# Performance work log

Measured on AMD Instinct MI355X. Metric: run time of the kernel, lower is better.

Reference implementation:

```python
import jax, jax.numpy as jnp
import numpy as np

K = 3  # involution kernel size


def dwconv3x3(x, w, b):
    # x: [B,C,H,W], w: [C,1,3,3] (depthwise, groups=C), b: [C]
    y = jax.lax.conv_general_dilated(
        x, w, window_strides=(1, 1), padding='SAME',
        dimension_numbers=('NCHW', 'OIHW', 'NCHW'),
        feature_group_count=x.shape[1])
    return y + b[None, :, None, None]


def conv1x1(x, w, b):
    # x: [B,C,H,W], w: [O,C], b: [O]
    return jnp.einsum('oc,bchw->bohw', w, x) + b[None, :, None, None]


def extract_patches(x):
    # x: [B,C,H,W] -> [B,C,K*K,H,W], zero-padded 'same' 3x3 neighborhoods
    B, C, H, W = x.shape
    p = (K - 1) // 2
    xp = jnp.pad(x, ((0, 0), (0, 0), (p, p), (p, p)))
    return jnp.stack([xp[:, :, i:i + H, j:j + W]
                      for i in range(K) for j in range(K)], axis=2)


def involution(x, w_red, b_red, w_span, b_span):
    # dynamic per-pixel kernels: [B, K*K, H, W]
    kern = conv1x1(jax.nn.relu(conv1x1(x, w_red, b_red)), w_span, b_span)
    patches = extract_patches(x)                 # [B,C,KK,H,W]
    return jnp.einsum('bkhw,bckhw->bchw', kern, patches)


def setup_inputs() -> dict:
    key = jax.random.key(0)
    ks = jax.random.split(key, 10)
    dim, red = 256, 64  # reduction ratio 4
    B, H, W = 8, 64, 64
    s = 0.05
    return {
        'x': jax.random.normal(ks[0], (B, dim, H, W), jnp.float32),
        'w_in': jax.random.normal(ks[1], (dim, 1, 3, 3), jnp.float32) * s,
        'b_in': jax.random.normal(ks[2], (dim,), jnp.float32) * s,
        'w_red': jax.random.normal(ks[3], (red, dim), jnp.float32) * s,
        'b_red': jax.random.normal(ks[4], (red,), jnp.float32) * s,
        'w_span': jax.random.normal(ks[5], (K * K, red), jnp.float32) * s,
        'b_span': jax.random.normal(ks[6], (K * K,), jnp.float32) * s,
        'w_out': jax.random.normal(ks[7], (dim, 1, 3, 3), jnp.float32) * s,
        'b_out': jax.random.normal(ks[8], (dim,), jnp.float32) * s,
    }


def reference(x, w_in, b_in, w_red, b_red, w_span, b_span, w_out, b_out):
    x = dwconv3x3(x, w_in, b_in)
    x = involution(x, w_red, b_red, w_span, b_span)
    x = dwconv3x3(x, w_out, b_out)
    return x
```

## Files before the change

### kernel.cpp

```cpp
#include <hip/hip_runtime.h>

#define BB 8
#define CC 256
#define HH 64
#define WW 64
#define RED 64
#define HW 4096
#define AST 72
#define LSF 68
#define LSH 72

typedef __attribute__((ext_vector_type(8))) short s8v;
typedef __attribute__((ext_vector_type(4))) float f4v;

__device__ __forceinline__ unsigned short f2bf(float f) {
    unsigned u = __float_as_uint(f);
    u += 0x7fff + ((u >> 16) & 1);
    return (unsigned short)(u >> 16);
}
__device__ __forceinline__ float b2f(unsigned short u) {
    return __uint_as_float(((unsigned)u) << 16);
}

__global__ __launch_bounds__(256) void build_wtf(const float* __restrict__ w_red,
                                                 unsigned short* __restrict__ wtf) {
    int e = blockIdx.x * 256 + threadIdx.x;
    int j = e & 7, l = (e >> 3) & 63, nt = (e >> 9) & 3, kbg = e >> 11;
    int o = nt * 16 + (l & 15);
    int c = kbg * 32 + ((l >> 4) & 3) * 8 + j;
    wtf[e] = f2bf(w_red[o * CC + c]);
}

__global__ __launch_bounds__(256, 4) void dw_kern(const float* __restrict__ x,
                                                  const float* __restrict__ w_in,
                                                  const float* __restrict__ b_in,
                                                  const unsigned short* __restrict__ wtf,
                                                  const float* __restrict__ b_red,
                                                  const float* __restrict__ w_span,
                                                  const float* __restrict__ b_span,
                                                  float* __restrict__ kern,
                                                  unsigned short* __restrict__ x1g) {
    alignas(16) __shared__ char smem[8448 + 12288];
    unsigned short* xs = (unsigned short*)smem;
    float* r_lds = (float*)smem;
    float* wl    = (float*)(smem + 8448);
    float* part  = (float*)(smem + 8448);

    const int t    = threadIdx.x;
    const int bx   = blockIdx.x;
    const int band = bx & 7;
    const int idx  = bx >> 3;
    const int h    = band * 8 + (idx >> 1);
    const int wh   = idx & 1;
    const int b    = blockIdx.y;
    const int l  = t & 63;
    const int wv = t >> 6;
    const int mt = wv & 1, nh = wv >> 1;
    const int m0 = mt << 4;
    const int q  = t & 7;
    const int pl = q << 2;
    const int wg = (wh << 5) | pl;
    const int cr = t >> 3;

    #pragma unroll
    for (int j = 0; j < 9; j++) {
        int i = j * 256 + t;
        wl[(i / 9) * 12 + (i % 9)] = w_in[i];
    }
    wl[t * 12 + 9] = b_in[t];

    float4 pv[2][3]; float plf[2][3], prt[2][3];

    auto loadX = [&](int c0) {
        #pragma unroll
        for (int s = 0; s < 2; s++) {
            const int cc = c0 + s * 32 + cr;
            const float* xp = x + ((size_t)(b * CC + cc)) * HW;
            #pragma unroll
            for (int ky = 0; ky < 3; ky++) {
                int hh = h + ky - 1;
                if (hh < 0 || hh >= HH) {
                    pv[s][ky] = make_float4(0.f, 0.f, 0.f, 0.f);
                    plf[s][ky] = 0.f; prt[s][ky] = 0.f;
                    continue;
                }
                const float* row = xp + hh * WW + wg;
                pv[s][ky]  = *(const float4*)row;
                plf[s][ky] = (wg > 0)      ? row[-1] : 0.f;
                prt[s][ky] = (wg + 4 < WW) ? row[4]  : 0.f;
            }
        }
    };
    auto computeA = [&](int c0) {
        #pragma unroll
        for (int s = 0; s < 2; s++) {
            const int cl = s * 32 + cr;
            const int cc = c0 + cl;
            const float* wp = wl + cc * 12;
            float4 wa = *(const float4*)wp;
            float4 wb = *(const float4*)(wp + 4);
            float2 wc = *(const float2*)(wp + 8);
            float4 a4 = make_float4(wc.y, wc.y, wc.y, wc.y);
            const float kw[9] = {wa.x, wa.y, wa.z, wa.w, wb.x, wb.y, wb.z, wb.w, wc.x};
            #pragma unroll
            for (int ky = 0; ky < 3; ky++) {
                float4 v = pv[s][ky];
                float lf = plf[s][ky], rt = prt[s][ky];
                float k0 = kw[ky * 3 + 0], k1 = kw[ky * 3 + 1], k2 = kw[ky * 3 + 2];
                a4.x = fmaf(k0, lf,  a4.x); a4.y = fmaf(k0, v.x, a4.y);
                a4.z = fmaf(k0, v.y, a4.z); a4.w = fmaf(k0, v.z, a4.w);
                a4.x = fmaf(k1, v.x, a4.x); a4.y = fmaf(k1, v.y, a4.y);
                a4.z = fmaf(k1, v.z, a4.z); a4.w = fmaf(k1, v.w, a4.w);
                a4.x = fmaf(k2, v.y, a4.x); a4.y = fmaf(k2, v.z, a4.y);
                a4.z = fmaf(k2, v.w, a4.z); a4.w = fmaf(k2, rt,  a4.w);
            }
            ushort4 pk;
            pk.x = f2bf(a4.x); pk.y = f2bf(a4.y);
            pk.z = f2bf(a4.z); pk.w = f2bf(a4.w);
            xs[(pl + 0) * AST + cl] = pk.x;
            xs[(pl + 1) * AST + cl] = pk.y;
            xs[(pl + 2) * AST + cl] = pk.z;
            xs[(pl + 3) * AST + cl] = pk.w;
            *(ushort4*)(x1g + ((size_t)(b * CC + cc)) * HW + h * WW + wg) = pk;
        }
    };

    s8v bfr[2][2];
    auto loadB = [&](int k) {
        #pragma unroll
        for (int kb = 0; kb < 2; kb++)
            #pragma unroll
            for (int ntl = 0; ntl < 2; ntl++) {
                int nt = (nh << 1) + ntl;
                int kbg = (k << 1) + kb;
                bfr[kb][ntl] = *(const s8v*)(wtf + (((kbg * 4 + nt) * 64 + l) << 3));
            }
    };

    f4v acc[2] = {{0.f, 0.f, 0.f, 0.f}, {0.f, 0.f, 0.f, 0.f}};

    loadX(0); loadB(0);
    __syncthreads();
    for (int k = 0; k < 4; k++) {
        computeA(k << 6);
        if (k < 3) loadX((k + 1) << 6);
        __syncthreads();
        #pragma unroll
        for (int kb = 0; kb < 2; kb++) {
            const unsigned short* ap =
                xs + (m0 + (l & 15)) * AST + (kb << 5) + ((l >> 4) & 3) * 8;
            s8v av = *(const s8v*)ap;
            #pragma unroll
            for (int ntl = 0; ntl < 2; ntl++)
                acc[ntl] = __builtin_amdgcn_mfma_f32_16x16x32_bf16(
                    av, bfr[kb][ntl], acc[ntl], 0, 0, 0);
        }
        if (k < 3) loadB(k + 1);
        __syncthreads();
    }

    #pragma unroll
    for (int ntl = 0; ntl < 2; ntl++) {
        int o = ((nh << 1) + ntl) * 16 + (l & 15);
        int pxr = m0 + ((l >> 4) & 3) * 4;
        #pragma unroll
        for (int i = 0; i < 4; i++)
            r_lds[o * 33 + pxr + i] = acc[ntl][i];
    }
    __syncthreads();

    const int px = t & 31;
    const int og = t >> 5;
    const int o0 = og << 3;
    float kk[9];
    #pragma unroll
    for (int j = 0; j < 9; j++) kk[j] = 0.f;
    #pragma unroll
    for (int i = 0; i < 8; i++) {
        float r = fmaxf(r_lds[(o0 + i) * 33 + px] + b_red[o0 + i], 0.f);
        #pragma unroll
        for (int j = 0; j < 9; j++) kk[j] = fmaf(w_span[j * RED + o0 + i], r, kk[j]);
    }
    __syncthreads();
    #pragma unroll
    for (int j = 0; j < 9; j++) part[(og * 9 + j) * 32 + px] = kk[j];
    __syncthreads();

    float* kp = kern + (size_t)b * 9 * HW + h * WW + (wh << 5) + px;
    const int jj = t >> 5;
    {
        float s = b_span[jj];
        #pragma unroll
        for (int g = 0; g < 8; g++) s += part[(g * 9 + jj) * 32 + px];
        kp[jj * HW] = s;
    }
    if (t < 32) {
        float s = b_span[8];
        #pragma unroll
        for (int g = 0; g < 8; g++) s += part[(g * 9 + 8) * 32 + px];
        kp[8 * HW] = s;
    }
}

__global__ __launch_bounds__(256) void invol_dw(const unsigned short* __restrict__ x1g,
                                                const float* __restrict__ kern,
                                                const float* __restrict__ w_out,
                                                const float* __restrict__ b_out,
                                                float* __restrict__ out) {
    __shared__ unsigned short x1s[HH * LSH];
    __shared__ float res[HH * LSF];
    const int t  = threadIdx.x;
    const int q  = t & 15;
    const int w0 = q << 2;
    const int r  = t >> 4;
    const int c = blockIdx.x, b = blockIdx.y;

    {
        const unsigned short* xp = x1g + ((size_t)(b * CC + c)) * HW;
        const int hl = t >> 2;
        const int wl2 = (t & 3) << 4;
        *(s8v*)&x1s[hl * LSH + wl2]     = *(const s8v*)(xp + hl * WW + wl2);
        *(s8v*)&x1s[hl * LSH + wl2 + 8] = *(const s8v*)(xp + hl * WW + wl2 + 8);
    }
    __syncthreads();

    const float* kp = kern + (size_t)b * 9 * HW;
    #pragma unroll
    for (int i = 0; i < 4; i++) {
        int h  = r + (i << 4);
        int hw = h * WW + w0;
        float4 acc = make_float4(0.f, 0.f, 0.f, 0.f);
        #pragma unroll
        for (int ky = 0; ky < 3; ky++) {
            int hh = h + ky - 1;
            if (hh < 0 || hh >= HH) continue;
            const unsigned short* row = &x1s[hh * LSH + w0];
            float vx = b2f(row[0]), vy = b2f(row[1]);
            float vz = b2f(row[2]), vw = b2f(row[3]);
            float lf = (w0 > 0)      ? b2f(row[-1]) : 0.f;
            float rt = (w0 + 4 < WW) ? b2f(row[4])  : 0.f;
            float4 k0 = *(const float4*)(kp + (ky * 3 + 0) * HW + hw);
            float4 k1 = *(const float4*)(kp + (ky * 3 + 1) * HW + hw);
            float4 k2 = *(const float4*)(kp + (ky * 3 + 2) * HW + hw);
            acc.x = fmaf(k0.x, lf, acc.x); acc.y = fmaf(k0.y, vx, acc.y);
            acc.z = fmaf(k0.z, vy, acc.z); acc.w = fmaf(k0.w, vz, acc.w);
            acc.x = fmaf(k1.x, vx, acc.x); acc.y = fmaf(k1.y, vy, acc.y);
            acc.z = fmaf(k1.z, vz, acc.z); acc.w = fmaf(k1.w, vw, acc.w);
            acc.x = fmaf(k2.x, vy, acc.x); acc.y = fmaf(k2.y, vz, acc.y);
            acc.z = fmaf(k2.z, vw, acc.z); acc.w = fmaf(k2.w, rt, acc.w);
        }
        *(float4*)&res[h * LSF + w0] = acc;
    }
    __syncthreads();

    const float* wp = w_out + c * 9;
    const float bb = b_out[c];
    float* op = out + ((size_t)(b * CC + c)) * HW;
    #pragma unroll
    for (int i = 0; i < 4; i++) {
        int h = r + (i << 4);
        float4 acc = make_float4(bb, bb, bb, bb);
        #pragma unroll
        for (int ky = 0; ky < 3; ky++) {
            int hh = h + ky - 1;
            if (hh < 0 || hh >= HH) continue;
            const float* row = &res[hh * LSF + w0];
            float4 v = *(const float4*)row;
            float lf = (w0 > 0)      ? row[-1] : 0.f;
            float rt = (w0 + 4 < WW) ? row[4]  : 0.f;
            float k0 = wp[ky * 3 + 0], k1 = wp[ky * 3 + 1], k2 = wp[ky * 3 + 2];
            acc.x = fmaf(k0, lf,  acc.x); acc.y = fmaf(k0, v.x, acc.y);
            acc.z = fmaf(k0, v.y, acc.z); acc.w = fmaf(k0, v.z, acc.w);
            acc.x = fmaf(k1, v.x, acc.x); acc.y = fmaf(k1, v.y, acc.y);
            acc.z = fmaf(k1, v.z, acc.z); acc.w = fmaf(k1, v.w, acc.w);
            acc.x = fmaf(k2, v.y, acc.x); acc.y = fmaf(k2, v.z, acc.y);
            acc.z = fmaf(k2, v.w, acc.z); acc.w = fmaf(k2, rt,  acc.w);
        }
        *(float4*)(op + h * WW + w0) = acc;
    }
}

extern "C" void kernel_launch(void* const* d_in, const int* in_sizes, int n_in,
                              void* d_out, int out_size, void* d_ws, size_t ws_size,
                              hipStream_t stream) {
    const float* x      = (const float*)d_in[0];
    const float* w_in   = (const float*)d_in[1];
    const float* b_in   = (const float*)d_in[2];
    const float* w_red  = (const float*)d_in[3];
    const float* b_red  = (const float*)d_in[4];
    const float* w_span = (const float*)d_in[5];
    const float* b_span = (const float*)d_in[6];
    const float* w_out  = (const float*)d_in[7];
    const float* b_out  = (const float*)d_in[8];
    float* out = (float*)d_out;

    float* kern = (float*)d_ws;
    unsigned short* x1g = (unsigned short*)(kern + (size_t)BB * 9 * HW);
    unsigned short* wtf = x1g + (size_t)BB * CC * HW;

    build_wtf<<<64, 256, 0, stream>>>(w_red, wtf);
    dw_kern<<<dim3(128, BB), 256, 0, stream>>>(x, w_in, b_in, wtf, b_red,
                                               w_span, b_span, kern, x1g);
    invol_dw<<<dim3(CC, BB), 256, 0, stream>>>(x1g, kern, w_out, b_out, out);
}
```

Before: 138.1 us.

## Halve dw_kern pixel tile, shrink LDS, store involution intermediate as bf16

dw_kern now processes 16 pixels per block instead of 32, so it launches twice as many blocks. Each wave handles one MFMA tile, LDS use is reduced, and launch bounds are raised to allow more resident blocks, aiming at better latency hiding. invol_dw stores its intermediate involution result in LDS as bf16 instead of fp32, halving that buffer so more blocks fit per CU. The trade-offs are more redundant halo loads and duplicated weight staging per block, plus an extra bf16 rounding step before the output depthwise conv, which reduces precision.

```diff
diff --git a/kernel.cpp b/kernel.cpp
--- a/kernel.cpp
+++ b/kernel.cpp
@@ -7,8 +7,8 @@
 #define RED 64
 #define HW 4096
 #define AST 72
-#define LSF 68
 #define LSH 72
+#define WLS 10
 
 typedef __attribute__((ext_vector_type(8))) short s8v;
 typedef __attribute__((ext_vector_type(4))) float f4v;
@@ -31,7 +31,7 @@
     wtf[e] = f2bf(w_red[o * CC + c]);
 }
 
-__global__ __launch_bounds__(256, 4) void dw_kern(const float* __restrict__ x,
+__global__ __launch_bounds__(256, 8) void dw_kern(const float* __restrict__ x,
                                                   const float* __restrict__ w_in,
                                                   const float* __restrict__ b_in,
                                                   const unsigned short* __restrict__ wtf,
@@ -40,104 +40,89 @@
                                                   const float* __restrict__ b_span,
                                                   float* __restrict__ kern,
                                                   unsigned short* __restrict__ x1g) {
-    alignas(16) __shared__ char smem[8448 + 12288];
+    alignas(16) __shared__ char smem[4608 + 10240];
     unsigned short* xs = (unsigned short*)smem;
     float* r_lds = (float*)smem;
-    float* wl    = (float*)(smem + 8448);
-    float* part  = (float*)(smem + 8448);
+    float* wl    = (float*)(smem + 4608);
+    float* part  = (float*)(smem + 4608);
 
     const int t    = threadIdx.x;
     const int bx   = blockIdx.x;
     const int band = bx & 7;
     const int idx  = bx >> 3;
-    const int h    = band * 8 + (idx >> 1);
-    const int wh   = idx & 1;
+    const int h    = band * 8 + (idx >> 2);
+    const int qh   = idx & 3;
     const int b    = blockIdx.y;
     const int l  = t & 63;
     const int wv = t >> 6;
-    const int mt = wv & 1, nh = wv >> 1;
-    const int m0 = mt << 4;
-    const int q  = t & 7;
+    const int q  = t & 3;
     const int pl = q << 2;
-    const int wg = (wh << 5) | pl;
-    const int cr = t >> 3;
+    const int wg = (qh << 4) | pl;
+    const int cr = t >> 2;
 
     #pragma unroll
     for (int j = 0; j < 9; j++) {
         int i = j * 256 + t;
-        wl[(i / 9) * 12 + (i % 9)] = w_in[i];
-    }
-    wl[t * 12 + 9] = b_in[t];
-
-    float4 pv[2][3]; float plf[2][3], prt[2][3];
+        wl[(i / 9) * WLS + (i % 9)] = w_in[i];
+    }
+    wl[t * WLS + 9] = b_in[t];
+
+    float4 pv[3]; float plf[3], prt[3];
 
     auto loadX = [&](int c0) {
-        #pragma unroll
-        for (int s = 0; s < 2; s++) {
-            const int cc = c0 + s * 32 + cr;
-            const float* xp = x + ((size_t)(b * CC + cc)) * HW;
-            #pragma unroll
-            for (int ky = 0; ky < 3; ky++) {
-                int hh = h + ky - 1;
-                if (hh < 0 || hh >= HH) {
-                    pv[s][ky] = make_float4(0.f, 0.f, 0.f, 0.f);
-                    plf[s][ky] = 0.f; prt[s][ky] = 0.f;
-                    continue;
-                }
-                const float* row = xp + hh * WW + wg;
-                pv[s][ky]  = *(const float4*)row;
-                plf[s][ky] = (wg > 0)      ? row[-1] : 0.f;
-                prt[s][ky] = (wg + 4 < WW) ? row[4]  : 0.f;
+        const int cc = c0 + cr;
+        const float* xp = x + ((size_t)(b * CC + cc)) * HW;
+        #pragma unroll
+        for (int ky = 0; ky < 3; ky++) {
+            int hh = h + ky - 1;
+            if (hh < 0 || hh >= HH) {
+                pv[ky] = make_float4(0.f, 0.f, 0.f, 0.f);
+                plf[ky] = 0.f; prt[ky] = 0.f;
+                continue;
             }
+            const float* row = xp + hh * WW + wg;
+            pv[ky]  = *(const float4*)row;
+            plf[ky] = (wg > 0)      ? row[-1] : 0.f;
+            prt[ky] = (wg + 4 < WW) ? row[4]  : 0.f;
         }
     };
     auto computeA = [&](int c0) {
-        #pragma unroll
-        for (int s = 0; s < 2; s++) {
-            const int cl = s * 32 + cr;
-            const int cc = c0 + cl;
-            const float* wp = wl + cc * 12;
-            float4 wa = *(const float4*)wp;
-            float4 wb = *(const float4*)(wp + 4);
-            float2 wc = *(const float2*)(wp + 8);
-            float4 a4 = make_float4(wc.y, wc.y, wc.y, wc.y);
-            const float kw[9] = {wa.x, wa.y, wa.z, wa.w, wb.x, wb.y, wb.z, wb.w, wc.x};
-            #pragma unroll
-            for (int ky = 0; ky < 3; ky++) {
-                float4 v = pv[s][ky];
-                float lf = plf[s][ky], rt = prt[s][ky];
-                float k0 = kw[ky * 3 + 0], k1 = kw[ky * 3 + 1], k2 = kw[ky * 3 + 2];
-                a4.x = fmaf(k0, lf,  a4.x); a4.y = fmaf(k0, v.x, a4.y);
-                a4.z = fmaf(k0, v.y, a4.z); a4.w = fmaf(k0, v.z, a4.w);
-                a4.x = fmaf(k1, v.x, a4.x); a4.y = fmaf(k1, v.y, a4.y);
-                a4.z = fmaf(k1, v.z, a4.z); a4.w = fmaf(k1, v.w, a4.w);
-                a4.x = fmaf(k2, v.y, a4.x); a4.y = fmaf(k2, v.z, a4.y);
-                a4.z = fmaf(k2, v.w, a4.z); a4.w = fmaf(k2, rt,  a4.w);
-            }
-            ushort4 pk;
-            pk.x = f2bf(a4.x); pk.y = f2bf(a4.y);
-            pk.z = f2bf(a4.z); pk.w = f2bf(a4.w);
-            xs[(pl + 0) * AST + cl] = pk.x;
-            xs[(pl + 1) * AST + cl] = pk.y;
-            xs[(pl + 2) * AST + cl] = pk.z;
-            xs[(pl + 3) * AST + cl] = pk.w;
-            *(ushort4*)(x1g + ((size_t)(b * CC + cc)) * HW + h * WW + wg) = pk;
-        }
+        const int cc = c0 + cr;
+        const float* wp = wl + cc * WLS;
+        const float bb = wp[9];
+        float4 a4 = make_float4(bb, bb, bb, bb);
+        #pragma unroll
+        for (int ky = 0; ky < 3; ky++) {
+            float4 v = pv[ky];
+            float lf = plf[ky], rt = prt[ky];
+            float k0 = wp[ky * 3 + 0], k1 = wp[ky * 3 + 1], k2 = wp[ky * 3 + 2];
+            a4.x = fmaf(k0, lf,  a4.x); a4.y = fmaf(k0, v.x, a4.y);
+            a4.z = fmaf(k0, v.y, a4.z); a4.w = fmaf(k0, v.z, a4.w);
+            a4.x = fmaf(k1, v.x, a4.x); a4.y = fmaf(k1, v.y, a4.y);
+            a4.z = fmaf(k1, v.z, a4.z); a4.w = fmaf(k1, v.w, a4.w);
+            a4.x = fmaf(k2, v.y, a4.x); a4.y = fmaf(k2, v.z, a4.y);
+            a4.z = fmaf(k2, v.w, a4.z); a4.w = fmaf(k2, rt,  a4.w);
+        }
+        ushort4 pk;
+        pk.x = f2bf(a4.x); pk.y = f2bf(a4.y);
+        pk.z = f2bf(a4.z); pk.w = f2bf(a4.w);
+        xs[(pl + 0) * AST + cr] = pk.x;
+        xs[(pl + 1) * AST + cr] = pk.y;
+        xs[(pl + 2) * AST + cr] = pk.z;
+        xs[(pl + 3) * AST + cr] = pk.w;
+        *(ushort4*)(x1g + ((size_t)(b * CC + cc)) * HW + h * WW + wg) = pk;
     };
 
-    s8v bfr[2][2];
+    s8v bfr[2];
     auto loadB = [&](int k) {
         #pragma unroll
-        for (int kb = 0; kb < 2; kb++)
-            #pragma unroll
-            for (int ntl = 0; ntl < 2; ntl++) {
-                int nt = (nh << 1) + ntl;
-                int kbg = (k << 1) + kb;
-                bfr[kb][ntl] = *(const s8v*)(wtf + (((kbg * 4 + nt) * 64 + l) << 3));
-            }
+        for (int kb = 0; kb < 2; kb++) {
+            int kbg = (k << 1) + kb;
+            bfr[kb] = *(const s8v*)(wtf + (((kbg * 4 + wv) * 64 + l) << 3));
+        }
     };
 
-    f4v acc[2] = {{0.f, 0.f, 0.f, 0.f}, {0.f, 0.f, 0.f, 0.f}};
+    f4v acc = {0.f, 0.f, 0.f, 0.f};
 
     loadX(0); loadB(0);
     __syncthreads();
@@ -148,67 +133,56 @@
         #pragma unroll
         for (int kb = 0; kb < 2; kb++) {
             const unsigned short* ap =
-                xs + (m0 + (l & 15)) * AST + (kb << 5) + ((l >> 4) & 3) * 8;
+                xs + (l & 15) * AST + (kb << 5) + ((l >> 4) & 3) * 8;
             s8v av = *(const s8v*)ap;
-            #pragma unroll
-            for (int ntl = 0; ntl < 2; ntl++)
-                acc[ntl] = __builtin_amdgcn_mfma_f32_16x16x32_bf16(
-                    av, bfr[kb][ntl], acc[ntl], 0, 0, 0);
+            acc = __builtin_amdgcn_mfma_f32_16x16x32_bf16(av, bfr[kb], acc, 0, 0, 0);
         }
         if (k < 3) loadB(k + 1);
         __syncthreads();
     }
 
-    #pragma unroll
-    for (int ntl = 0; ntl < 2; ntl++) {
-        int o = ((nh << 1) + ntl) * 16 + (l & 15);
-        int pxr = m0 + ((l >> 4) & 3) * 4;
+    {
+        int o = (wv << 4) + (l & 15);
+        int pxr = ((l >> 4) & 3) * 4;
         #pragma unroll
         for (int i = 0; i < 4; i++)
-            r_lds[o * 33 + pxr + i] = acc[ntl][i];
-    }
-    __syncthreads();
-
-    const int px = t & 31;
-    const int og = t >> 5;
-    const int o0 = og << 3;
+            r_lds[o * 17 + pxr + i] = acc[i];
+    }
+    __syncthreads();
+
+    const int px = t & 15;
+    const int og = t >> 4;
+    const int o0 = og << 2;
     float kk[9];
     #pragma unroll
     for (int j = 0; j < 9; j++) kk[j] = 0.f;
     #pragma unroll
-    for (int i = 0; i < 8; i++) {
-        float r = fmaxf(r_lds[(o0 + i) * 33 + px] + b_red[o0 + i], 0.f);
+    for (int i = 0; i < 4; i++) {
+        float r = fmaxf(r_lds[(o0 + i) * 17 + px] + b_red[o0 + i], 0.f);
         #pragma unroll
         for (int j = 0; j < 9; j++) kk[j] = fmaf(w_span[j * RED + o0 + i], r, kk[j]);
     }
     __syncthreads();
     #pragma unroll
-    for (int j = 0; j < 9; j++) part[(og * 9 + j) * 32 + px] = kk[j];
-    __syncthreads();
-
-    float* kp = kern + (size_t)b * 9 * HW + h * WW + (wh << 5) + px;
-    const int jj = t >> 5;
-    {
+    for (int j = 0; j < 9; j++) part[(og * 9 + j) * 16 + px] = kk[j];
+    __syncthreads();
+
+    if (t < 144) {
+        const int jj = t >> 4;
         float s = b_span[jj];
         #pragma unroll
-        for (int g = 0; g < 8; g++) s += part[(g * 9 + jj) * 32 + px];
-        kp[jj * HW] = s;
-    }
-    if (t < 32) {
-        float s = b_span[8];
-        #pragma unroll
-        for (int g = 0; g < 8; g++) s += part[(g * 9 + 8) * 32 + px];
-        kp[8 * HW] = s;
-    }
-}
-
-__global__ __launch_bounds__(256) void invol_dw(const unsigned short* __restrict__ x1g,
-                                                const float* __restrict__ kern,
-                                                const float* __restrict__ w_out,
-                                                const float* __restrict__ b_out,
-                                                float* __restrict__ out) {
+        for (int g = 0; g < 16; g++) s += part[(g * 9 + jj) * 16 + px];
+        kern[(size_t)b * 9 * HW + jj * HW + h * WW + (qh << 4) + px] = s;
+    }
+}
+
+__global__ __launch_bounds__(256, 8) void invol_dw(const unsigned short* __restrict__ x1g,
+                                                   const float* __restrict__ kern,
+                                                   const float* __restrict__ w_out,
+                                                   const float* __restrict__ b_out,
+                                                   float* __restrict__ out) {
     __shared__ unsigned short x1s[HH * LSH];
-    __shared__ float res[HH * LSF];
+    __shared__ unsigned short res[HH * LSH];
     const int t  = threadIdx.x;
     const int q  = t & 15;
     const int w0 = q << 2;
@@ -249,7 +223,10 @@
             acc.x = fmaf(k2.x, vy, acc.x); acc.y = fmaf(k2.y, vz, acc.y);
             acc.z = fmaf(k2.z, vw, acc.z); acc.w = fmaf(k2.w, rt, acc.w);
         }
-        *(float4*)&res[h * LSF + w0] = acc;
+        ushort4 pk;
+        pk.x = f2bf(acc.x); pk.y = f2bf(acc.y);
+        pk.z = f2bf(acc.z); pk.w = f2bf(acc.w);
+        *(ushort4*)&res[h * LSH + w0] = pk;
     }
     __syncthreads();
 
@@ -264,17 +241,18 @@
         for (int ky = 0; ky < 3; ky++) {
             int hh = h + ky - 1;
             if (hh < 0 || hh >= HH) continue;
-            const float* row = &res[hh * LSF + w0];
-            float4 v = *(const float4*)row;
-            float lf = (w0 > 0)      ? row[-1] : 0.f;
-            float rt = (w0 + 4 < WW) ? row[4]  : 0.f;
+            const unsigned short* row = &res[hh * LSH + w0];
+            float vx = b2f(row[0]), vy = b2f(row[1]);
+            float vz = b2f(row[2]), vw = b2f(row[3]);
+            float lf = (w0 > 0)      ? b2f(row[-1]) : 0.f;
+            float rt = (w0 + 4 < WW) ? b2f(row[4])  : 0.f;
             float k0 = wp[ky * 3 + 0], k1 = wp[ky * 3 + 1], k2 = wp[ky * 3 + 2];
-            acc.x = fmaf(k0, lf,  acc.x); acc.y = fmaf(k0, v.x, acc.y);
-            acc.z = fmaf(k0, v.y, acc.z); acc.w = fmaf(k0, v.z, acc.w);
-            acc.x = fmaf(k1, v.x, acc.x); acc.y = fmaf(k1, v.y, acc.y);
-            acc.z = fmaf(k1, v.z, acc.z); acc.w = fmaf(k1, v.w, acc.w);
-            acc.x = fmaf(k2, v.y, acc.x); acc.y = fmaf(k2, v.z, acc.y);
-            acc.z = fmaf(k2, v.w, acc.z); acc.w = fmaf(k2, rt,  acc.w);
+            acc.x = fmaf(k0, lf, acc.x); acc.y = fmaf(k0, vx, acc.y);
+            acc.z = fmaf(k0, vy, acc.z); acc.w = fmaf(k0, vz, acc.w);
+            acc.x = fmaf(k1, vx, acc.x); acc.y = fmaf(k1, vy, acc.y);
+            acc.z = fmaf(k1, vz, acc.z); acc.w = fmaf(k1, vw, acc.w);
+            acc.x = fmaf(k2, vy, acc.x); acc.y = fmaf(k2, vz, acc.y);
+            acc.z = fmaf(k2, vw, acc.z); acc.w = fmaf(k2, rt, acc.w);
         }
         *(float4*)(op + h * WW + w0) = acc;
     }
@@ -299,7 +277,7 @@
     unsigned short* wtf = x1g + (size_t)BB * CC * HW;
 
     build_wtf<<<64, 256, 0, stream>>>(w_red, wtf);
-    dw_kern<<<dim3(128, BB), 256, 0, stream>>>(x, w_in, b_in, wtf, b_red,
+    dw_kern<<<dim3(256, BB), 256, 0, stream>>>(x, w_in, b_in, wtf, b_red,
                                                w_span, b_span, kern, x1g);
     invol_dw<<<dim3(CC, BB), 256, 0, stream>>>(x1g, kern, w_out, b_out, out);
 }
```

Result: slower. 162.5 us (+17.6%).

## Coalesce x1 stores via LDS staging, shuffle halos, bf16 intermediate in invol_dw

Applied to the files above, without the earlier changes.

The first kernel now stages each bf16 x1 tile in shared memory and writes it to global as 16-byte vectors at the end, instead of issuing scattered 8-byte stores per channel. It also gets horizontal halo values through lane shuffles rather than extra global loads, and caches w_span, b_red and b_span in LDS. The second kernel keeps its intermediate result in LDS as bf16, halving that buffer so launch bounds can allow 8 blocks. The bf16 intermediate adds rounding error, and the first kernel's extra LDS use may lower its occupancy.

```diff
diff --git a/kernel.cpp b/kernel.cpp
--- a/kernel.cpp
+++ b/kernel.cpp
@@ -7,8 +7,9 @@
 #define RED 64
 #define HW 4096
 #define AST 72
-#define LSF 68
+#define XST 40
 #define LSH 72
+#define WLS 10
 
 typedef __attribute__((ext_vector_type(8))) short s8v;
 typedef __attribute__((ext_vector_type(4))) float f4v;
@@ -40,11 +41,15 @@
                                                   const float* __restrict__ b_span,
                                                   float* __restrict__ kern,
                                                   unsigned short* __restrict__ x1g) {
-    alignas(16) __shared__ char smem[8448 + 12288];
-    unsigned short* xs = (unsigned short*)smem;
-    float* r_lds = (float*)smem;
-    float* wl    = (float*)(smem + 8448);
-    float* part  = (float*)(smem + 8448);
+    alignas(16) __shared__ char smem[8448 + 5120 + 10240 + 2640];
+    unsigned short* xs  = (unsigned short*)smem;
+    float* r_lds        = (float*)smem;
+    unsigned short* xst = (unsigned short*)(smem + 8448);
+    float* wl           = (float*)(smem + 13568);
+    float* part         = (float*)(smem + 13568);
+    float* ws_l         = (float*)(smem + 23808);
+    float* br_l         = ws_l + 576;
+    float* bs_l         = br_l + 64;
 
     const int t    = threadIdx.x;
     const int bx   = blockIdx.x;
@@ -65,11 +70,15 @@
     #pragma unroll
     for (int j = 0; j < 9; j++) {
         int i = j * 256 + t;
-        wl[(i / 9) * 12 + (i % 9)] = w_in[i];
-    }
-    wl[t * 12 + 9] = b_in[t];
-
-    float4 pv[2][3]; float plf[2][3], prt[2][3];
+        wl[(i / 9) * WLS + (i % 9)] = w_in[i];
+    }
+    wl[t * WLS + 9] = b_in[t];
+    ws_l[t]       = w_span[t];
+    ws_l[256 + t] = w_span[256 + t];
+    if (t < 64) { ws_l[512 + t] = w_span[512 + t]; br_l[t] = b_red[t]; }
+    if (t < 9)  bs_l[t] = b_span[t];
+
+    float4 pv[2][3]; float phal[2][3];
 
     auto loadX = [&](int c0) {
         #pragma unroll
@@ -81,13 +90,15 @@
                 int hh = h + ky - 1;
                 if (hh < 0 || hh >= HH) {
                     pv[s][ky] = make_float4(0.f, 0.f, 0.f, 0.f);
-                    plf[s][ky] = 0.f; prt[s][ky] = 0.f;
+                    phal[s][ky] = 0.f;
                     continue;
                 }
                 const float* row = xp + hh * WW + wg;
-                pv[s][ky]  = *(const float4*)row;
-                plf[s][ky] = (wg > 0)      ? row[-1] : 0.f;
-                prt[s][ky] = (wg + 4 < WW) ? row[4]  : 0.f;
+                pv[s][ky] = *(const float4*)row;
+                float hv = 0.f;
+                if (q == 0) { if (wg > 0) hv = row[-1]; }
+                else if (q == 7) { if (wg + 4 < WW) hv = row[4]; }
+                phal[s][ky] = hv;
             }
         }
     };
@@ -96,17 +107,17 @@
         for (int s = 0; s < 2; s++) {
             const int cl = s * 32 + cr;
             const int cc = c0 + cl;
-            const float* wp = wl + cc * 12;
-            float4 wa = *(const float4*)wp;
-            float4 wb = *(const float4*)(wp + 4);
-            float2 wc = *(const float2*)(wp + 8);
-            float4 a4 = make_float4(wc.y, wc.y, wc.y, wc.y);
-            const float kw[9] = {wa.x, wa.y, wa.z, wa.w, wb.x, wb.y, wb.z, wb.w, wc.x};
+            const float* wp = wl + cc * WLS;
+            const float bb = wp[9];
+            float4 a4 = make_float4(bb, bb, bb, bb);
             #pragma unroll
             for (int ky = 0; ky < 3; ky++) {
                 float4 v = pv[s][ky];
-                float lf = plf[s][ky], rt = prt[s][ky];
-                float k0 = kw[ky * 3 + 0], k1 = kw[ky * 3 + 1], k2 = kw[ky * 3 + 2];
+                float lf = __shfl_up(v.w, 1);
+                if (q == 0) lf = phal[s][ky];
+                float rt = __shfl_down(v.x, 1);
+                if (q == 7) rt = phal[s][ky];
+                float k0 = wp[ky * 3 + 0], k1 = wp[ky * 3 + 1], k2 = wp[ky * 3 + 2];
                 a4.x = fmaf(k0, lf,  a4.x); a4.y = fmaf(k0, v.x, a4.y);
                 a4.z = fmaf(k0, v.y, a4.z); a4.w = fmaf(k0, v.z, a4.w);
                 a4.x = fmaf(k1, v.x, a4.x); a4.y = fmaf(k1, v.y, a4.y);
@@ -121,7 +132,7 @@
             xs[(pl + 1) * AST + cl] = pk.y;
             xs[(pl + 2) * AST + cl] = pk.z;
             xs[(pl + 3) * AST + cl] = pk.w;
-            *(ushort4*)(x1g + ((size_t)(b * CC + cc)) * HW + h * WW + wg) = pk;
+            *(ushort4*)&xst[cl * XST + pl] = pk;
         }
     };
 
@@ -138,6 +149,9 @@
     };
 
     f4v acc[2] = {{0.f, 0.f, 0.f, 0.f}, {0.f, 0.f, 0.f, 0.f}};
+    int4 x1r[4];
+    const int c2  = t >> 2;
+    const int px2 = (t & 3) << 3;
 
     loadX(0); loadB(0);
     __syncthreads();
@@ -155,6 +169,7 @@
                 acc[ntl] = __builtin_amdgcn_mfma_f32_16x16x32_bf16(
                     av, bfr[kb][ntl], acc[ntl], 0, 0, 0);
         }
+        x1r[k] = *(const int4*)&xst[c2 * XST + px2];
         if (k < 3) loadB(k + 1);
         __syncthreads();
     }
@@ -177,9 +192,9 @@
     for (int j = 0; j < 9; j++) kk[j] = 0.f;
     #pragma unroll
     for (int i = 0; i < 8; i++) {
-        float r = fmaxf(r_lds[(o0 + i) * 33 + px] + b_red[o0 + i], 0.f);
-        #pragma unroll
-        for (int j = 0; j < 9; j++) kk[j] = fmaf(w_span[j * RED + o0 + i], r, kk[j]);
+        float r = fmaxf(r_lds[(o0 + i) * 33 + px] + br_l[o0 + i], 0.f);
+        #pragma unroll
+        for (int j = 0; j < 9; j++) kk[j] = fmaf(ws_l[j * 64 + o0 + i], r, kk[j]);
     }
     __syncthreads();
     #pragma unroll
@@ -189,26 +204,33 @@
     float* kp = kern + (size_t)b * 9 * HW + h * WW + (wh << 5) + px;
     const int jj = t >> 5;
     {
-        float s = b_span[jj];
+        float s = bs_l[jj];
         #pragma unroll
         for (int g = 0; g < 8; g++) s += part[(g * 9 + jj) * 32 + px];
         kp[jj * HW] = s;
     }
     if (t < 32) {
-        float s = b_span[8];
+        float s = bs_l[8];
         #pragma unroll
         for (int g = 0; g < 8; g++) s += part[(g * 9 + 8) * 32 + px];
         kp[8 * HW] = s;
     }
-}
-
-__global__ __launch_bounds__(256) void invol_dw(const unsigned short* __restrict__ x1g,
-                                                const float* __restrict__ kern,
-                                                const float* __restrict__ w_out,
-                                                const float* __restrict__ b_out,
-                                                float* __restrict__ out) {
+
+    #pragma unroll
+    for (int k = 0; k < 4; k++) {
+        unsigned short* dst = x1g + ((size_t)(b * CC + (k << 6) + c2)) * HW
+                            + h * WW + (wh << 5) + px2;
+        *(int4*)dst = x1r[k];
+    }
+}
+
+__global__ __launch_bounds__(256, 8) void invol_dw(const unsigned short* __restrict__ x1g,
+                                                   const float* __restrict__ kern,
+                                                   const float* __restrict__ w_out,
+                                                   const float* __restrict__ b_out,
+                                                   float* __restrict__ out) {
     __shared__ unsigned short x1s[HH * LSH];
-    __shared__ float res[HH * LSF];
+    __shared__ unsigned short res[HH * LSH];
     const int t  = threadIdx.x;
     const int q  = t & 15;
     const int w0 = q << 2;
@@ -249,7 +271,10 @@
             acc.x = fmaf(k2.x, vy, acc.x); acc.y = fmaf(k2.y, vz, acc.y);
             acc.z = fmaf(k2.z, vw, acc.z); acc.w = fmaf(k2.w, rt, acc.w);
         }
-        *(float4*)&res[h * LSF + w0] = acc;
+        ushort4 pk;
+        pk.x = f2bf(acc.x); pk.y = f2bf(acc.y);
+        pk.z = f2bf(acc.z); pk.w = f2bf(acc.w);
+        *(ushort4*)&res[h * LSH + w0] = pk;
     }
     __syncthreads();
 
@@ -264,17 +289,18 @@
         for (int ky = 0; ky < 3; ky++) {
             int hh = h + ky - 1;
             if (hh < 0 || hh >= HH) continue;
-            const float* row = &res[hh * LSF + w0];
-            float4 v = *(const float4*)row;
-            float lf = (w0 > 0)      ? row[-1] : 0.f;
-            float rt = (w0 + 4 < WW) ? row[4]  : 0.f;
+            const unsigned short* row = &res[hh * LSH + w0];
+            float vx = b2f(row[0]), vy = b2f(row[1]);
+            float vz = b2f(row[2]), vw = b2f(row[3]);
+            float lf = (w0 > 0)      ? b2f(row[-1]) : 0.f;
+            float rt = (w0 + 4 < WW) ? b2f(row[4])  : 0.f;
             float k0 = wp[ky * 3 + 0], k1 = wp[ky * 3 + 1], k2 = wp[ky * 3 + 2];
-            acc.x = fmaf(k0, lf,  acc.x); acc.y = fmaf(k0, v.x, acc.y);
-            acc.z = fmaf(k0, v.y, acc.z); acc.w = fmaf(k0, v.z, acc.w);
-            acc.x = fmaf(k1, v.x, acc.x); acc.y = fmaf(k1, v.y, acc.y);
-            acc.z = fmaf(k1, v.z, acc.z); acc.w = fmaf(k1, v.w, acc.w);
-            acc.x = fmaf(k2, v.y, acc.x); acc.y = fmaf(k2, v.z, acc.y);
-            acc.z = fmaf(k2, v.w, acc.z); acc.w = fmaf(k2, rt,  acc.w);
+            acc.x = fmaf(k0, lf, acc.x); acc.y = fmaf(k0, vx, acc.y);
+            acc.z = fmaf(k0, vy, acc.z); acc.w = fmaf(k0, vz, acc.w);
+            acc.x = fmaf(k1, vx, acc.x); acc.y = fmaf(k1, vy, acc.y);
+            acc.z = fmaf(k1, vz, acc.z); acc.w = fmaf(k1, vw, acc.w);
+            acc.x = fmaf(k2, vy, acc.x); acc.y = fmaf(k2, vz, acc.y);
+            acc.z = fmaf(k2, vw, acc.z); acc.w = fmaf(k2, rt, acc.w);
         }
         *(float4*)(op + h * WW + w0) = acc;
     }
```

After: 143.0 us. 3.6% more time.
